# Performance work log

Measured on AMD Instinct MI355X. Metric: run time of the kernel, lower is better.

The kernel has to match this reference:

```python
import jax, jax.numpy as jnp
import numpy as np

S = 100   # n_pred_samples
B = 64    # batch
DIMS = [784, 512, 512, 10]


def setup_inputs() -> dict:
    key = jax.random.key(0)
    ks = jax.random.split(key, 16)
    d = {}
    d["inputs"] = jax.random.normal(ks[0], (B, DIMS[0]), dtype=jnp.float32)
    d["task_id"] = 0
    # variational params: means ~ 0.1*N(0,1), logvars constant -6 (as in module init)
    d["wm0"] = jax.random.normal(ks[1], (DIMS[0], DIMS[1])) * 0.1
    d["wv0"] = jnp.full((DIMS[0], DIMS[1]), -6.0, jnp.float32)
    d["bm0"] = jnp.full((DIMS[1],), 0.1, jnp.float32)
    d["bv0"] = jnp.full((DIMS[1],), -6.0, jnp.float32)
    d["wm1"] = jax.random.normal(ks[2], (DIMS[1], DIMS[2])) * 0.1
    d["wv1"] = jnp.full((DIMS[1], DIMS[2]), -6.0, jnp.float32)
    d["bm1"] = jnp.full((DIMS[2],), 0.1, jnp.float32)
    d["bv1"] = jnp.full((DIMS[2],), -6.0, jnp.float32)
    d["wml"] = jax.random.normal(ks[3], (DIMS[2], DIMS[3])) * 0.1
    d["wvl"] = jnp.full((DIMS[2], DIMS[3]), -6.0, jnp.float32)
    d["bml"] = jnp.full((DIMS[3],), 0.1, jnp.float32)
    d["bvl"] = jnp.full((DIMS[3],), -6.0, jnp.float32)
    # reparameterization noise (passed explicitly for determinism)
    d["we0"] = jax.random.normal(ks[4], (S, DIMS[0], DIMS[1]), dtype=jnp.float32)
    d["be0"] = jax.random.normal(ks[5], (S, 1, DIMS[1]), dtype=jnp.float32)
    d["we1"] = jax.random.normal(ks[6], (S, DIMS[1], DIMS[2]), dtype=jnp.float32)
    d["be1"] = jax.random.normal(ks[7], (S, 1, DIMS[2]), dtype=jnp.float32)
    d["wel"] = jax.random.normal(ks[8], (S, DIMS[2], DIMS[3]), dtype=jnp.float32)
    d["bel"] = jax.random.normal(ks[9], (S, 1, DIMS[3]), dtype=jnp.float32)
    return d


def _sample(eps, logvar, mean):
    # reparameterization: eps * exp(0.5*logvar) + mean
    return eps * jnp.exp(0.5 * logvar) + mean


def reference(inputs, task_id, wm0, wv0, bm0, bv0, wm1, wv1, bm1, bv1,
              wml, wvl, bml, bvl, we0, be0, we1, be1, wel, bel):
    # activations: [S, B, D]
    act = jnp.broadcast_to(inputs[None], (S,) + inputs.shape)
    # hidden layer 0
    W0 = _sample(we0, wv0, wm0)          # [S, D0, D1]
    b0 = _sample(be0, bv0, bm0)          # [S, 1, D1]
    act = jax.nn.relu(jnp.einsum('sbi,sio->sbo', act, W0) + b0)
    # hidden layer 1
    W1 = _sample(we1, wv1, wm1)
    b1 = _sample(be1, bv1, bm1)
    act = jax.nn.relu(jnp.einsum('sbi,sio->sbo', act, W1) + b1)
    # last (task-specific) layer: original does broadcast-mul + sum over dim 2,
    # which is exactly a batched matmul — expressed here as an einsum
    Wl = _sample(wel, wvl, wml)          # [S, D2, O]
    bl = _sample(bel, bvl, bml)          # [S, 1, O]
    logits = jnp.einsum('sbh,sho->sbo', act, Wl) + bl   # [S, B, O]
    return logits
```

## Files before the change

kernel.cpp:

```cpp
#include <hip/hip_runtime.h>
#include <hip/hip_bf16.h>


typedef __bf16 bf16x8 __attribute__((ext_vector_type(8)));
typedef float f32x4 __attribute__((ext_vector_type(4)));

#define NSAMP 100
#define BATCH 64
#define D0 784
#define D1 512
#define D2 512
#define DOUT 10
#define K0PAD 800
#define RSB 40

__device__ __forceinline__ unsigned short f2bf(float f) {
    __bf16 b = (__bf16)f;
    return __builtin_bit_cast(unsigned short, b);
}
__device__ __forceinline__ float bf_hi(unsigned int u) {
    return __builtin_bit_cast(float, u & 0xffff0000u);
}
__device__ __forceinline__ float bf_lo(unsigned int u) {
    return __builtin_bit_cast(float, u << 16);
}

union FragU { uint4 q; bf16x8 v; };

#define XB_N   (BATCH * K0PAD)
#define PS0_N  (D0 * D1)
#define PS1_N  (D1 * D2)
#define SGL_N  (D2 * DOUT)
#define B0_N   (NSAMP * D1)
#define B1_N   (NSAMP * D2)
#define BL_N   (NSAMP * DOUT)
#define PREP_TOTAL (XB_N + PS0_N + PS1_N + SGL_N + B0_N + B1_N + BL_N)

__global__ __launch_bounds__(256) void prep(
    const float* __restrict__ inputs,
    const float* __restrict__ wv0, const float* __restrict__ wm0,
    const float* __restrict__ wv1, const float* __restrict__ wm1,
    const float* __restrict__ wvl,
    const float* __restrict__ be0, const float* __restrict__ bv0, const float* __restrict__ bm0,
    const float* __restrict__ be1, const float* __restrict__ bv1, const float* __restrict__ bm1,
    const float* __restrict__ bel, const float* __restrict__ bvl, const float* __restrict__ bml,
    unsigned short* __restrict__ Xb,
    unsigned int* __restrict__ psm0, unsigned int* __restrict__ psm1,
    float* __restrict__ sigmal,
    float* __restrict__ bias0, float* __restrict__ bias1, float* __restrict__ biasl)
{
    int i = blockIdx.x * 256 + threadIdx.x;
    if (i < XB_N) {
        int m = i / K0PAD, k = i % K0PAD;
        float v = (k < D0) ? inputs[m * D0 + k] : 0.f;
        Xb[i] = f2bf(v);
        return;
    }
    i -= XB_N;
    if (i < PS0_N) {
        unsigned int sg = f2bf(__expf(0.5f * wv0[i]));
        unsigned int mn = f2bf(wm0[i]);
        psm0[i] = (sg << 16) | mn;
        return;
    }
    i -= PS0_N;
    if (i < PS1_N) {
        unsigned int sg = f2bf(__expf(0.5f * wv1[i]));
        unsigned int mn = f2bf(wm1[i]);
        psm1[i] = (sg << 16) | mn;
        return;
    }
    i -= PS1_N;
    if (i < SGL_N) { sigmal[i] = __expf(0.5f * wvl[i]); return; }
    i -= SGL_N;
    if (i < B0_N) { int n = i % D1; bias0[i] = fmaf(be0[i], __expf(0.5f * bv0[n]), bm0[n]); return; }
    i -= B0_N;
    if (i < B1_N) { int n = i % D2; bias1[i] = fmaf(be1[i], __expf(0.5f * bv1[n]), bm1[n]); return; }
    i -= B1_N;
    if (i < BL_N) { int o = i % DOUT; biasl[i] = fmaf(bel[i], __expf(0.5f * bvl[o]), bml[o]); return; }
}

__global__ __launch_bounds__(64) void gemm_wave(
    const unsigned short* __restrict__ A, int lda, long aStride,
    const float* __restrict__ eps, long eStride,
    const unsigned int* __restrict__ psm,
    int KT, int Kvalid,
    const float* __restrict__ bias,
    void* __restrict__ outp, int outBf16)
{
    __shared__ unsigned short smB[32 * RSB];

    const int bx = blockIdx.x;
    const int s  = bx >> 4;
    const int n0 = (bx & 15) << 5;
    const int l  = threadIdx.x;
    const int fr = l & 15, quad = l >> 4;
    const int kg = l >> 3;
    const int ng = l & 7;

    const unsigned short* aP = A + (long)s * aStride + (long)fr * lda + quad * 8;
    const float* eB        = eps + (long)s * eStride + n0 + 4 * ng;
    const unsigned int* pB = psm + n0 + 4 * ng;

    f32x4 acc[4][2] = {};

    float4 ea0[4], ea1[4];
    uint4  pa0[4], pa1[4], aa0[4], aa1[4];

    auto loadAll = [&](int kt, float4* ea, uint4* pa, uint4* aa) {
        const int kb = kt * 32;
#pragma unroll
        for (int mi = 0; mi < 4; ++mi)
            aa[mi] = *reinterpret_cast<const uint4*>(aP + (long)(mi * 16) * lda + kb);
#pragma unroll
        for (int j = 0; j < 4; ++j) {
            const int row = kb + 4 * kg + j;
            const bool ok = row < Kvalid;
            const long off = (long)(ok ? row : 0) * 512;
            float4 e = *reinterpret_cast<const float4*>(eB + off);
            uint4  p = *reinterpret_cast<const uint4*>(pB + off);
            if (!ok) { e = float4{0.f, 0.f, 0.f, 0.f}; p = uint4{0u, 0u, 0u, 0u}; }
            ea[j] = e; pa[j] = p;
        }
    };

    auto stage = [&](const float4* ea, const uint4* pa) {
        float w[4][4];
#pragma unroll
        for (int j = 0; j < 4; ++j) {
            w[j][0] = fmaf(ea[j].x, bf_hi(pa[j].x), bf_lo(pa[j].x));
            w[j][1] = fmaf(ea[j].y, bf_hi(pa[j].y), bf_lo(pa[j].y));
            w[j][2] = fmaf(ea[j].z, bf_hi(pa[j].z), bf_lo(pa[j].z));
            w[j][3] = fmaf(ea[j].w, bf_hi(pa[j].w), bf_lo(pa[j].w));
        }
#pragma unroll
        for (int i = 0; i < 4; ++i) {
            uint2 d;
            d.x = (unsigned)f2bf(w[0][i]) | ((unsigned)f2bf(w[1][i]) << 16);
            d.y = (unsigned)f2bf(w[2][i]) | ((unsigned)f2bf(w[3][i]) << 16);
            *reinterpret_cast<uint2*>(&smB[(4 * ng + i) * RSB + 4 * kg]) = d;
        }
    };

    auto compute = [&](const uint4* aa) {
        FragU bf0, bf1;
        bf0.q = *reinterpret_cast<const uint4*>(&smB[fr * RSB + quad * 8]);
        bf1.q = *reinterpret_cast<const uint4*>(&smB[(16 + fr) * RSB + quad * 8]);
#pragma unroll
        for (int mi = 0; mi < 4; ++mi) {
            FragU af; af.q = aa[mi];
            acc[mi][0] = __builtin_amdgcn_mfma_f32_16x16x32_bf16(af.v, bf0.v, acc[mi][0], 0, 0, 0);
            acc[mi][1] = __builtin_amdgcn_mfma_f32_16x16x32_bf16(af.v, bf1.v, acc[mi][1], 0, 0, 0);
        }
    };

    loadAll(0, ea0, pa0, aa0);
    int kt = 0;
    for (; kt + 2 <= KT; kt += 2) {
        loadAll(kt + 1, ea1, pa1, aa1);
        stage(ea0, pa0);
        compute(aa0);
        if (kt + 2 < KT) loadAll(kt + 2, ea0, pa0, aa0);
        stage(ea1, pa1);
        compute(aa1);
    }
    if (kt < KT) { stage(ea0, pa0); compute(aa0); }

    const float bv0v = bias[(long)s * 512 + n0 + fr];
    const float bv1v = bias[(long)s * 512 + n0 + 16 + fr];
    const long outBase = (long)s * BATCH * 512;
#pragma unroll
    for (int mi = 0; mi < 4; ++mi) {
#pragma unroll
        for (int ni = 0; ni < 2; ++ni) {
            const float bv = ni ? bv1v : bv0v;
            const int col = n0 + ni * 16 + fr;
#pragma unroll
            for (int r = 0; r < 4; ++r) {
                const int row = mi * 16 + quad * 4 + r;
                float v = fmaxf(acc[mi][ni][r] + bv, 0.f);
                const long idx = outBase + (long)row * 512 + col;
                if (outBf16) ((unsigned short*)outp)[idx] = f2bf(v);
                else         ((float*)outp)[idx] = v;
            }
        }
    }
}

__global__ __launch_bounds__(320) void last_layer(
    const float* __restrict__ act2,
    const float* __restrict__ wel,
    const float* __restrict__ sigmal,
    const float* __restrict__ wml,
    const float* __restrict__ biasl,
    float* __restrict__ out)
{
    __shared__ float smW[D2 * DOUT];
    const int s = blockIdx.x;
    const int t = threadIdx.x;
    const float* we = wel + (long)s * D2 * DOUT;
    for (int i = t; i < D2 * DOUT; i += 320)
        smW[i] = fmaf(we[i], sigmal[i], wml[i]);
    __syncthreads();

    const int m  = t / 5;
    const int op = t % 5;
    const float* a = act2 + ((long)s * BATCH + m) * D2;
    float acc0 = 0.f, acc1 = 0.f;
#pragma unroll 4
    for (int k = 0; k < D2; k += 4) {
        float4 av = *reinterpret_cast<const float4*>(a + k);
        acc0 = fmaf(av.x, smW[(k + 0) * DOUT + op], acc0);
        acc0 = fmaf(av.y, smW[(k + 1) * DOUT + op], acc0);
        acc0 = fmaf(av.z, smW[(k + 2) * DOUT + op], acc0);
        acc0 = fmaf(av.w, smW[(k + 3) * DOUT + op], acc0);
        acc1 = fmaf(av.x, smW[(k + 0) * DOUT + op + 5], acc1);
        acc1 = fmaf(av.y, smW[(k + 1) * DOUT + op + 5], acc1);
        acc1 = fmaf(av.z, smW[(k + 2) * DOUT + op + 5], acc1);
        acc1 = fmaf(av.w, smW[(k + 3) * DOUT + op + 5], acc1);
    }
    const long ob = ((long)s * BATCH + m) * DOUT;
    out[ob + op]     = acc0 + biasl[s * DOUT + op];
    out[ob + op + 5] = acc1 + biasl[s * DOUT + op + 5];
}

extern "C" void kernel_launch(void* const* d_in, const int* in_sizes, int n_in,
                              void* d_out, int out_size, void* d_ws, size_t ws_size,
                              hipStream_t stream)
{
    const float* inputs = (const float*)d_in[0];
    const float* wm0 = (const float*)d_in[2];
    const float* wv0 = (const float*)d_in[3];
    const float* bm0 = (const float*)d_in[4];
    const float* bv0 = (const float*)d_in[5];
    const float* wm1 = (const float*)d_in[6];
    const float* wv1 = (const float*)d_in[7];
    const float* bm1 = (const float*)d_in[8];
    const float* bv1 = (const float*)d_in[9];
    const float* wml = (const float*)d_in[10];
    const float* wvl = (const float*)d_in[11];
    const float* bml = (const float*)d_in[12];
    const float* bvl = (const float*)d_in[13];
    const float* we0 = (const float*)d_in[14];
    const float* be0 = (const float*)d_in[15];
    const float* we1 = (const float*)d_in[16];
    const float* be1 = (const float*)d_in[17];
    const float* wel = (const float*)d_in[18];
    const float* bel = (const float*)d_in[19];

    char* w = (char*)d_ws;
    unsigned short* Xb  = (unsigned short*)w; w += (size_t)XB_N * 2;
    unsigned int* psm0  = (unsigned int*)w;   w += (size_t)PS0_N * 4;
    unsigned int* psm1  = (unsigned int*)w;   w += (size_t)PS1_N * 4;
    float* sigmal = (float*)w; w += (size_t)SGL_N * 4;
    float* bias0  = (float*)w; w += (size_t)B0_N * 4;
    float* bias1  = (float*)w; w += (size_t)B1_N * 4;
    float* biasl  = (float*)w; w += (size_t)BL_N * 4;
    unsigned short* act1 = (unsigned short*)w; w += (size_t)NSAMP * BATCH * D1 * 2;
    float* act2 = (float*)w; w += (size_t)NSAMP * BATCH * D2 * 4;

    prep<<<dim3((PREP_TOTAL + 255) / 256), 256, 0, stream>>>(
        inputs, wv0, wm0, wv1, wm1, wvl,
        be0, bv0, bm0, be1, bv1, bm1, bel, bvl, bml,
        Xb, psm0, psm1, sigmal, bias0, bias1, biasl);

    gemm_wave<<<dim3(NSAMP * 16), 64, 0, stream>>>(
        Xb, K0PAD, 0L, we0, (long)D0 * D1, psm0,
        K0PAD / 32, D0, bias0, (void*)act1, 1);

    gemm_wave<<<dim3(NSAMP * 16), 64, 0, stream>>>(
        act1, D1, (long)BATCH * D1, we1, (long)D1 * D2, psm1,
        D1 / 32, D1, bias1, (void*)act2, 0);

    last_layer<<<dim3(NSAMP), 320, 0, stream>>>(
        act2, wel, sigmal, wml, biasl, (float*)d_out);
}
```

Measured before the change: 406.9 us.

## Split-K GEMM across 256 full-width blocks with separate bias-ReLU reduction

Replaces the per-wave 32-column GEMM grid with 1024-thread blocks that each cover all 512 output columns of one sample over a slice of K. Samples are split three or two ways along K so the grid comes to 256 blocks. Partial sums go to a workspace and a new reduction kernel adds them with bias and ReLU. This aims to balance work across CUs and raise occupancy. In exchange it writes and re-reads large fp32 partial buffers, adds two kernel launches, and drops the register double-buffered prefetch in favour of block-wide syncs.

Result: slower. 415.6 us (+2.1%).

```diff
diff --git a/kernel.cpp b/kernel.cpp
--- a/kernel.cpp
+++ b/kernel.cpp
@@ -13,6 +13,7 @@
 #define DOUT 10
 #define K0PAD 800
 #define RSB 40
+#define S3 56
 
 __device__ __forceinline__ unsigned short f2bf(float f) {
     __bf16 b = (__bf16)f;
@@ -25,7 +26,7 @@
     return __builtin_bit_cast(float, u << 16);
 }
 
-union FragU { uint4 q; bf16x8 v; };
+union FragU { uint4 q; uint2 d[2]; bf16x8 v; };
 
 #define XB_N   (BATCH * K0PAD)
 #define PS0_N  (D0 * D1)
@@ -80,110 +81,130 @@
     if (i < BL_N) { int o = i % DOUT; biasl[i] = fmaf(bel[i], __expf(0.5f * bvl[o]), bml[o]); return; }
 }
 
-__global__ __launch_bounds__(64) void gemm_wave(
+__global__ __launch_bounds__(1024) void gemm_full(
     const unsigned short* __restrict__ A, int lda, long aStride,
     const float* __restrict__ eps, long eStride,
     const unsigned int* __restrict__ psm,
-    int KT, int Kvalid,
-    const float* __restrict__ bias,
-    void* __restrict__ outp, int outBf16)
-{
-    __shared__ unsigned short smB[32 * RSB];
-
-    const int bx = blockIdx.x;
-    const int s  = bx >> 4;
-    const int n0 = (bx & 15) << 5;
-    const int l  = threadIdx.x;
-    const int fr = l & 15, quad = l >> 4;
-    const int kg = l >> 3;
-    const int ng = l & 7;
+    int KTtotal, int Kvalid,
+    float* __restrict__ partial)
+{
+    __shared__ unsigned short smB[16 * 32 * RSB];
+
+    const int b = blockIdx.x;
+    int s, c, ks;
+    if (b < S3 * 3) { s = b / 3; c = b - 3 * s; ks = 3; }
+    else            { int t = b - S3 * 3; s = S3 + (t >> 1); c = t & 1; ks = 2; }
+    const int base = KTtotal / ks, rem = KTtotal % ks;
+    const int kt0 = c * base + (c < rem ? c : rem);
+    const int ktn = base + (c < rem ? 1 : 0);
+
+    const int w    = threadIdx.x >> 6;
+    const int lane = threadIdx.x & 63;
+    const int fr = lane & 15, quad = lane >> 4;
+    const int kg = lane >> 3, ng = lane & 7;
+    const int n0 = w << 5;
 
     const unsigned short* aP = A + (long)s * aStride + (long)fr * lda + quad * 8;
     const float* eB        = eps + (long)s * eStride + n0 + 4 * ng;
     const unsigned int* pB = psm + n0 + 4 * ng;
+    unsigned short* smW = &smB[w * 32 * RSB];
 
     f32x4 acc[4][2] = {};
 
-    float4 ea0[4], ea1[4];
-    uint4  pa0[4], pa1[4], aa0[4], aa1[4];
-
-    auto loadAll = [&](int kt, float4* ea, uint4* pa, uint4* aa) {
+    for (int kt = kt0; kt < kt0 + ktn; ++kt) {
         const int kb = kt * 32;
+        __syncthreads();
+        uint4 aa[4];
 #pragma unroll
         for (int mi = 0; mi < 4; ++mi)
             aa[mi] = *reinterpret_cast<const uint4*>(aP + (long)(mi * 16) * lda + kb);
+        float4 e[4]; uint4 p[4];
 #pragma unroll
         for (int j = 0; j < 4; ++j) {
             const int row = kb + 4 * kg + j;
-            const bool ok = row < Kvalid;
-            const long off = (long)(ok ? row : 0) * 512;
-            float4 e = *reinterpret_cast<const float4*>(eB + off);
-            uint4  p = *reinterpret_cast<const uint4*>(pB + off);
-            if (!ok) { e = float4{0.f, 0.f, 0.f, 0.f}; p = uint4{0u, 0u, 0u, 0u}; }
-            ea[j] = e; pa[j] = p;
+            const bool okr = row < Kvalid;
+            const long off = (long)(okr ? row : 0) * 512;
+            float4 ev = *reinterpret_cast<const float4*>(eB + off);
+            uint4  pv = *reinterpret_cast<const uint4*>(pB + off);
+            if (!okr) { ev = float4{0.f,0.f,0.f,0.f}; pv = uint4{0u,0u,0u,0u}; }
+            e[j] = ev; p[j] = pv;
         }
-    };
-
-    auto stage = [&](const float4* ea, const uint4* pa) {
-        float w[4][4];
-#pragma unroll
-        for (int j = 0; j < 4; ++j) {
-            w[j][0] = fmaf(ea[j].x, bf_hi(pa[j].x), bf_lo(pa[j].x));
-            w[j][1] = fmaf(ea[j].y, bf_hi(pa[j].y), bf_lo(pa[j].y));
-            w[j][2] = fmaf(ea[j].z, bf_hi(pa[j].z), bf_lo(pa[j].z));
-            w[j][3] = fmaf(ea[j].w, bf_hi(pa[j].w), bf_lo(pa[j].w));
+        {
+            float t[4][4];
+#pragma unroll
+            for (int j = 0; j < 4; ++j) {
+                t[j][0] = fmaf(e[j].x, bf_hi(p[j].x), bf_lo(p[j].x));
+                t[j][1] = fmaf(e[j].y, bf_hi(p[j].y), bf_lo(p[j].y));
+                t[j][2] = fmaf(e[j].z, bf_hi(p[j].z), bf_lo(p[j].z));
+                t[j][3] = fmaf(e[j].w, bf_hi(p[j].w), bf_lo(p[j].w));
+            }
+#pragma unroll
+            for (int i = 0; i < 4; ++i) {
+                uint2 d;
+                d.x = (unsigned)f2bf(t[0][i]) | ((unsigned)f2bf(t[1][i]) << 16);
+                d.y = (unsigned)f2bf(t[2][i]) | ((unsigned)f2bf(t[3][i]) << 16);
+                *reinterpret_cast<uint2*>(&smW[(4 * ng + i) * RSB + 4 * kg]) = d;
+            }
         }
-#pragma unroll
-        for (int i = 0; i < 4; ++i) {
-            uint2 d;
-            d.x = (unsigned)f2bf(w[0][i]) | ((unsigned)f2bf(w[1][i]) << 16);
-            d.y = (unsigned)f2bf(w[2][i]) | ((unsigned)f2bf(w[3][i]) << 16);
-            *reinterpret_cast<uint2*>(&smB[(4 * ng + i) * RSB + 4 * kg]) = d;
-        }
-    };
-
-    auto compute = [&](const uint4* aa) {
+        __syncthreads();
         FragU bf0, bf1;
-        bf0.q = *reinterpret_cast<const uint4*>(&smB[fr * RSB + quad * 8]);
-        bf1.q = *reinterpret_cast<const uint4*>(&smB[(16 + fr) * RSB + quad * 8]);
+        bf0.q = *reinterpret_cast<const uint4*>(&smW[fr * RSB + quad * 8]);
+        bf1.q = *reinterpret_cast<const uint4*>(&smW[(16 + fr) * RSB + quad * 8]);
 #pragma unroll
         for (int mi = 0; mi < 4; ++mi) {
             FragU af; af.q = aa[mi];
             acc[mi][0] = __builtin_amdgcn_mfma_f32_16x16x32_bf16(af.v, bf0.v, acc[mi][0], 0, 0, 0);
             acc[mi][1] = __builtin_amdgcn_mfma_f32_16x16x32_bf16(af.v, bf1.v, acc[mi][1], 0, 0, 0);
         }
-    };
-
-    loadAll(0, ea0, pa0, aa0);
-    int kt = 0;
-    for (; kt + 2 <= KT; kt += 2) {
-        loadAll(kt + 1, ea1, pa1, aa1);
-        stage(ea0, pa0);
-        compute(aa0);
-        if (kt + 2 < KT) loadAll(kt + 2, ea0, pa0, aa0);
-        stage(ea1, pa1);
-        compute(aa1);
-    }
-    if (kt < KT) { stage(ea0, pa0); compute(aa0); }
-
-    const float bv0v = bias[(long)s * 512 + n0 + fr];
-    const float bv1v = bias[(long)s * 512 + n0 + 16 + fr];
-    const long outBase = (long)s * BATCH * 512;
-#pragma unroll
-    for (int mi = 0; mi < 4; ++mi) {
-#pragma unroll
-        for (int ni = 0; ni < 2; ++ni) {
-            const float bv = ni ? bv1v : bv0v;
-            const int col = n0 + ni * 16 + fr;
+    }
+
+    float* out = partial + ((long)s * 3 + c) * (64 * 512);
+#pragma unroll
+    for (int mi = 0; mi < 4; ++mi)
+#pragma unroll
+        for (int ni = 0; ni < 2; ++ni)
 #pragma unroll
             for (int r = 0; r < 4; ++r) {
                 const int row = mi * 16 + quad * 4 + r;
-                float v = fmaxf(acc[mi][ni][r] + bv, 0.f);
-                const long idx = outBase + (long)row * 512 + col;
-                if (outBf16) ((unsigned short*)outp)[idx] = f2bf(v);
-                else         ((float*)outp)[idx] = v;
+                const int col = n0 + ni * 16 + fr;
+                out[(long)row * 512 + col] = acc[mi][ni][r];
             }
-        }
+}
+
+__global__ __launch_bounds__(256) void reduce_bias_relu(
+    const float* __restrict__ partial,
+    const float* __restrict__ bias,
+    void* __restrict__ outp, int outBf16)
+{
+    const long total4 = (long)NSAMP * 64 * 512 / 4;
+    long i4 = (long)blockIdx.x * 256 + threadIdx.x;
+    if (i4 >= total4) return;
+    const long e0 = i4 * 4;
+    const int s    = (int)(e0 >> 15);
+    const int in_s = (int)(e0 & 32767);
+    const int n    = in_s & 511;
+    const int ks   = (s < S3) ? 3 : 2;
+
+    const float* p = partial + (long)s * 3 * 32768 + in_s;
+    float4 v  = *reinterpret_cast<const float4*>(p);
+    float4 v1 = *reinterpret_cast<const float4*>(p + 32768);
+    v.x += v1.x; v.y += v1.y; v.z += v1.z; v.w += v1.w;
+    if (ks == 3) {
+        float4 v2 = *reinterpret_cast<const float4*>(p + 65536);
+        v.x += v2.x; v.y += v2.y; v.z += v2.z; v.w += v2.w;
+    }
+    const float4 bv = *reinterpret_cast<const float4*>(bias + (long)s * 512 + n);
+    v.x = fmaxf(v.x + bv.x, 0.f);
+    v.y = fmaxf(v.y + bv.y, 0.f);
+    v.z = fmaxf(v.z + bv.z, 0.f);
+    v.w = fmaxf(v.w + bv.w, 0.f);
+    if (outBf16) {
+        uint2 d;
+        d.x = (unsigned)f2bf(v.x) | ((unsigned)f2bf(v.y) << 16);
+        d.y = (unsigned)f2bf(v.z) | ((unsigned)f2bf(v.w) << 16);
+        reinterpret_cast<uint2*>(outp)[i4] = d;
+    } else {
+        reinterpret_cast<float4*>(outp)[i4] = v;
     }
 }
 
@@ -257,20 +278,25 @@
     float* bias1  = (float*)w; w += (size_t)B1_N * 4;
     float* biasl  = (float*)w; w += (size_t)BL_N * 4;
     unsigned short* act1 = (unsigned short*)w; w += (size_t)NSAMP * BATCH * D1 * 2;
-    float* act2 = (float*)w; w += (size_t)NSAMP * BATCH * D2 * 4;
+    float* act2    = (float*)w; w += (size_t)NSAMP * BATCH * D2 * 4;
+    float* partial = (float*)w; w += (size_t)NSAMP * 3 * BATCH * 512 * 4;
 
     prep<<<dim3((PREP_TOTAL + 255) / 256), 256, 0, stream>>>(
         inputs, wv0, wm0, wv1, wm1, wvl,
         be0, bv0, bm0, be1, bv1, bm1, bel, bvl, bml,
         Xb, psm0, psm1, sigmal, bias0, bias1, biasl);
 
-    gemm_wave<<<dim3(NSAMP * 16), 64, 0, stream>>>(
-        Xb, K0PAD, 0L, we0, (long)D0 * D1, psm0,
-        K0PAD / 32, D0, bias0, (void*)act1, 1);
-
-    gemm_wave<<<dim3(NSAMP * 16), 64, 0, stream>>>(
-        act1, D1, (long)BATCH * D1, we1, (long)D1 * D2, psm1,
-        D1 / 32, D1, bias1, (void*)act2, 0);
+    const int RED_GRID = (NSAMP * BATCH * 512 / 4 + 255) / 256;
+
+    gemm_full<<<dim3(256), 1024, 0, stream>>>(
+        Xb, K0PAD, 0L, we0, (long)D0 * D1, psm0, K0PAD / 32, D0, partial);
+    reduce_bias_relu<<<dim3(RED_GRID), 256, 0, stream>>>(
+        partial, bias0, (void*)act1, 1);
+
+    gemm_full<<<dim3(256), 1024, 0, stream>>>(
+        act1, D1, (long)BATCH * D1, we1, (long)D1 * D2, psm1, D1 / 32, D1, partial);
+    reduce_bias_relu<<<dim3(RED_GRID), 256, 0, stream>>>(
+        partial, bias1, (void*)act2, 0);
 
     last_layer<<<dim3(NSAMP), 320, 0, stream>>>(
         act2, wel, sigmal, wml, biasl, (float*)d_out);
```
